# Performance work log

Measured on AMD Instinct MI355X. Metric: run time of the kernel, lower is better.

## Reference

```python
import jax, jax.numpy as jnp
import numpy as np

B, T, H = 32, 8192, 128

def setup_inputs() -> dict:
    key = jax.random.key(0)
    k1, k2, k3, k4, k5, k6 = jax.random.split(key, 6)
    stdv = 1.0 / np.sqrt(H)
    return {
        "hidden": jax.random.normal(k1, (B, H), jnp.float32),
        "encoder_outputs": jax.random.normal(k2, (T, B, H), jnp.float32),
        "len_seq": jax.random.randint(k3, (B,), 1, T + 1),  # valid lengths in [1, T]
        "W_attn": jax.random.normal(k4, (H, 2 * H), jnp.float32) * stdv,
        "b_attn": jnp.zeros((H,), jnp.float32),
        "v": jax.random.uniform(k5, (H,), jnp.float32, -stdv, stdv),
    }

def reference(hidden, encoder_outputs, len_seq, W_attn, b_attn, v):
    # hidden: [B,H]; encoder_outputs: [T,B,H]; len_seq: [B]
    T_ = encoder_outputs.shape[0]
    enc = jnp.transpose(encoder_outputs, (1, 0, 2))          # [B,T,H]
    h = jnp.broadcast_to(hidden[:, None, :], enc.shape)       # [B,T,H]
    # score(): relu(Linear(cat)) then v . energy
    energy = jax.nn.relu(jnp.concatenate([h, enc], axis=-1) @ W_attn.T + b_attn)  # [B,T,H]
    scores = jnp.einsum('bth,h->bt', energy, v)               # [B,T]
    # ragged masked softmax: softmax over first len_seq[i] positions, zeros after
    mask = jnp.arange(T_)[None, :] < len_seq[:, None]         # [B,T]
    attn = jax.nn.softmax(jnp.where(mask, scores, -jnp.inf), axis=1)
    attn = jnp.where(mask, attn, 0.0)
    return attn[:, None, :]                                   # [B,1,T]
```

## Files before the change

kernel.cpp:

```cpp
#include <hip/hip_runtime.h>
#include <hip/hip_bf16.h>

#define B 32
#define T 8192
#define H 128

typedef __attribute__((ext_vector_type(8)))  short short8_t;
typedef __attribute__((ext_vector_type(16))) float f32x16;

static __device__ __forceinline__ unsigned fbits(float x) { return __builtin_bit_cast(unsigned, x); }
static __device__ __forceinline__ float bfloat(unsigned u) { return __builtin_bit_cast(float, u); }

static __device__ __forceinline__ void pack4hi(const float4 f,
                                               unsigned& hi0, unsigned& hi1) {
    const unsigned u0 = fbits(f.x), u1 = fbits(f.y), u2 = fbits(f.z), u3 = fbits(f.w);
    hi0 = (u0 >> 16) | (u1 & 0xffff0000u);
    hi1 = (u2 >> 16) | (u3 & 0xffff0000u);
}

#define WPK_OFF  16384

__global__ void k_prep(const float* __restrict__ hidden,
                       const float* __restrict__ W_attn,
                       const float* __restrict__ b_attn,
                       float* __restrict__ u,
                       unsigned short* __restrict__ wpk) {
    const int tid = threadIdx.x;
    if (blockIdx.x < 32) {
        const int b = blockIdx.x;
        __shared__ float hrow[H];
        if (tid < H) hrow[tid] = hidden[b * H + tid];
        __syncthreads();
        if (tid < H) {
            const float* w = W_attn + (size_t)tid * (2 * H);
            float acc = b_attn[tid];
#pragma unroll
            for (int k = 0; k < H; ++k) acc = fmaf(w[k], hrow[k], acc);
            u[b * H + tid] = acc;
        }
    } else {
        const int idx  = (blockIdx.x - 32) * 256 + tid;
        const int s    = idx >> 8;
        const int m    = (idx >> 6) & 3;
        const int lane = idx & 63;
        const int h    = m * 32 + (lane & 31);
        const int k0   = s * 16 + (lane >> 5) * 8;
        const float* src = W_attn + (size_t)h * (2 * H) + H + k0;
        const int base = ((s * 4 + m) * 64 + lane) * 8;
#pragma unroll
        for (int e = 0; e < 8; ++e) {
            const float x = src[e];
            const unsigned ux = fbits(x);
            const unsigned hb = ux & 0xffff0000u;
            const float r = x - bfloat(hb);
            wpk[base + e]         = (unsigned short)(ux >> 16);
            wpk[16384 + base + e] = (unsigned short)(fbits(r) >> 16);
        }
    }
}

__global__ __launch_bounds__(512, 2) void k_scores_mfma(
    const float* __restrict__ enc,
    const float* __restrict__ u,
    const float* __restrict__ v,
    const unsigned short* __restrict__ wpk,
    float* __restrict__ scores)
{
    __shared__ uint2 hb[2][2048];
    __shared__ float cbuf[2][2][4][32];

    const int tid   = threadIdx.x;
    const int lane  = tid & 63;
    const int wid   = tid >> 6;
    const int tsel  = wid >> 2;
    const int mtile = wid & 3;
    const int l31   = lane & 31;
    const int kh    = lane >> 5;

    const int srow = tid >> 3;
    const int st8  = tid & 7;

    const int t0 = blockIdx.x * 32;
    const float4* enc4 = (const float4*)enc;

    short8_t w2hi[8], w2lo[8];
#pragma unroll
    for (int s = 0; s < 8; ++s) {
        const int fo = ((s * 4 + mtile) * 64 + lane) * 8;
        w2hi[s] = *(const short8_t*)(wpk + fo);
        w2lo[s] = *(const short8_t*)(wpk + 16384 + fo);
    }
    float4 uf[4], vv[4];
#pragma unroll
    for (int r4 = 0; r4 < 4; ++r4) {
        uf[r4] = *(const float4*)(u + l31 * H + mtile * 32 + r4 * 8 + kh * 4);
        vv[r4] = *(const float4*)(v + mtile * 32 + r4 * 8 + kh * 4);
    }

    float4 stg[4];
    {
        const float4* gs = enc4 + ((size_t)(t0 + 0) * 32 + srow) * 32;
#pragma unroll
        for (int i = 0; i < 4; ++i) stg[i] = gs[st8 + 8 * i];
#pragma unroll
        for (int i = 0; i < 4; ++i) {
            unsigned hi0, hi1;
            pack4hi(stg[i], hi0, hi1);
            const int p16 = st8 + 8 * i;
            const int idx = srow * 32 + (((p16 >> 1) + srow) & 15) * 2 + (p16 & 1);
            hb[0][idx] = make_uint2(hi0, hi1);
        }
        const float4* gs1 = enc4 + ((size_t)(t0 + 2) * 32 + srow) * 32;
#pragma unroll
        for (int i = 0; i < 4; ++i) stg[i] = gs1[st8 + 8 * i];
    }
    __syncthreads();

    const int rrow  = tsel * 32 + l31;
    const int rbase = rrow * 32;

#pragma unroll 1
    for (int q = 0; q < 16; ++q) {
        const int cur = q & 1, nxt = cur ^ 1;

        if (q < 15) {
#pragma unroll
            for (int i = 0; i < 4; ++i) {
                unsigned hi0, hi1;
                pack4hi(stg[i], hi0, hi1);
                const int p16 = st8 + 8 * i;
                const int idx = srow * 32 + (((p16 >> 1) + srow) & 15) * 2 + (p16 & 1);
                hb[nxt][idx] = make_uint2(hi0, hi1);
            }
        }
        if (q < 14) {
            const float4* gs = enc4 + ((size_t)(t0 + 2 * (q + 2)) * 32 + srow) * 32;
#pragma unroll
            for (int i = 0; i < 4; ++i) stg[i] = gs[st8 + 8 * i];
        }

        f32x16 acc;
#pragma unroll
        for (int r4 = 0; r4 < 4; ++r4) {
            acc[4 * r4 + 0] = uf[r4].x; acc[4 * r4 + 1] = uf[r4].y;
            acc[4 * r4 + 2] = uf[r4].z; acc[4 * r4 + 3] = uf[r4].w;
        }

#pragma unroll
        for (int s = 0; s < 8; ++s) {
            const int slot = (2 * s + kh + l31) & 15;
            const short8_t bh = *(const short8_t*)&hb[cur][rbase + slot * 2];
            acc = __builtin_amdgcn_mfma_f32_32x32x16_bf16(w2hi[s], bh, acc, 0, 0, 0);
            acc = __builtin_amdgcn_mfma_f32_32x32x16_bf16(w2lo[s], bh, acc, 0, 0, 0);
        }

        float psum = 0.f;
#pragma unroll
        for (int r4 = 0; r4 < 4; ++r4) {
            psum = fmaf(fmaxf(acc[4 * r4 + 0], 0.f), vv[r4].x, psum);
            psum = fmaf(fmaxf(acc[4 * r4 + 1], 0.f), vv[r4].y, psum);
            psum = fmaf(fmaxf(acc[4 * r4 + 2], 0.f), vv[r4].z, psum);
            psum = fmaf(fmaxf(acc[4 * r4 + 3], 0.f), vv[r4].w, psum);
        }
        psum += __shfl_xor(psum, 32);

        if (lane < 32) cbuf[cur][tsel][mtile][l31] = psum;

        __syncthreads();

        if (mtile == 0 && lane < 32) {
            const float r = cbuf[cur][tsel][0][l31] + cbuf[cur][tsel][1][l31]
                          + cbuf[cur][tsel][2][l31] + cbuf[cur][tsel][3][l31];
            scores[(size_t)l31 * T + (t0 + 2 * q + tsel)] = r;
        }
    }
}

#define SM_TPB 1024
#define SM_PER (T / SM_TPB)

__global__ __launch_bounds__(SM_TPB) void k_softmax(
    float* __restrict__ out, const int* __restrict__ len_seq)
{
    const int b    = blockIdx.x;
    const int tid  = threadIdx.x;
    const int lane = tid & 63;
    const int wid  = tid >> 6;
    const int len  = len_seq[b];
    float* s = out + (size_t)b * T;

    __shared__ float red[16];

    float val[SM_PER];
#pragma unroll
    for (int i = 0; i < SM_PER; ++i) val[i] = s[tid + i * SM_TPB];

    float m = -1e30f;
#pragma unroll
    for (int i = 0; i < SM_PER; ++i)
        if (tid + i * SM_TPB < len) m = fmaxf(m, val[i]);
#pragma unroll
    for (int off = 32; off >= 1; off >>= 1) m = fmaxf(m, __shfl_xor(m, off));
    if (lane == 0) red[wid] = m;
    __syncthreads();
    if (wid == 0) {
        float xv = (lane < 16) ? red[lane] : -1e30f;
#pragma unroll
        for (int off = 8; off >= 1; off >>= 1) xv = fmaxf(xv, __shfl_xor(xv, off));
        if (lane == 0) red[0] = xv;
    }
    __syncthreads();
    m = red[0];
    __syncthreads();

    float sum = 0.0f;
#pragma unroll
    for (int i = 0; i < SM_PER; ++i) {
        const int t = tid + i * SM_TPB;
        val[i] = (t < len) ? __expf(val[i] - m) : 0.0f;
        sum += val[i];
    }
#pragma unroll
    for (int off = 32; off >= 1; off >>= 1) sum += __shfl_xor(sum, off);
    if (lane == 0) red[wid] = sum;
    __syncthreads();
    if (wid == 0) {
        float xv = (lane < 16) ? red[lane] : 0.f;
#pragma unroll
        for (int off = 8; off >= 1; off >>= 1) xv += __shfl_xor(xv, off);
        if (lane == 0) red[0] = xv;
    }
    __syncthreads();
    const float inv = 1.0f / red[0];

#pragma unroll
    for (int i = 0; i < SM_PER; ++i) s[tid + i * SM_TPB] = val[i] * inv;
}

extern "C" void kernel_launch(void* const* d_in, const int* in_sizes, int n_in,
                              void* d_out, int out_size, void* d_ws, size_t ws_size,
                              hipStream_t stream) {
    const float* hidden = (const float*)d_in[0];
    const float* enc    = (const float*)d_in[1];
    const int*   len    = (const int*)d_in[2];
    const float* W      = (const float*)d_in[3];
    const float* bb     = (const float*)d_in[4];
    const float* v      = (const float*)d_in[5];

    float* out  = (float*)d_out;
    float* u_ws = (float*)d_ws;
    unsigned short* wpk = (unsigned short*)((char*)d_ws + WPK_OFF);

    k_prep<<<40, 256, 0, stream>>>(hidden, W, bb, u_ws, wpk);
    k_scores_mfma<<<256, 512, 0, stream>>>(enc, u_ws, v, wpk, out);
    k_softmax<<<B, SM_TPB, 0, stream>>>(out, len);
}
```

Measured before the change: 36.06 us.

## Fuse online softmax statistics into score kernel and widen final normalization grid

The score kernel now keeps running max and sum-of-exponentials per batch row (online softmax) for its time slice and writes per-block partials to workspace. A new final kernel merges the 256 partials per row and normalizes scores using 256 blocks instead of 32 large ones. This removes the separate max/sum reduction passes over the scores and spreads the final pass across more CUs. The cost is extra exp work inside the score loop, a serialized per-lane update, and a partial-merge step with extra exp calls.

```diff
diff --git a/kernel.cpp b/kernel.cpp
--- a/kernel.cpp
+++ b/kernel.cpp
@@ -19,6 +19,7 @@
 }
 
 #define WPK_OFF  16384
+#define PART_OFF 81920
 
 __global__ void k_prep(const float* __restrict__ hidden,
                        const float* __restrict__ W_attn,
@@ -64,10 +65,13 @@
     const float* __restrict__ u,
     const float* __restrict__ v,
     const unsigned short* __restrict__ wpk,
-    float* __restrict__ scores)
+    const int* __restrict__ len_seq,
+    float* __restrict__ scores,
+    float* __restrict__ part)
 {
     __shared__ uint2 hb[2][2048];
     __shared__ float cbuf[2][2][4][32];
+    __shared__ float pm[2][32], ps[2][32];
 
     const int tid   = threadIdx.x;
     const int lane  = tid & 63;
@@ -96,6 +100,7 @@
         uf[r4] = *(const float4*)(u + l31 * H + mtile * 32 + r4 * 8 + kh * 4);
         vv[r4] = *(const float4*)(v + mtile * 32 + r4 * 8 + kh * 4);
     }
+    const int lenb = len_seq[l31];
 
     float4 stg[4];
     {
@@ -118,6 +123,8 @@
 
     const int rrow  = tsel * 32 + l31;
     const int rbase = rrow * 32;
+
+    float m_run = -1e30f, s_run = 0.0f;
 
 #pragma unroll 1
     for (int q = 0; q < 16; ++q) {
@@ -171,70 +178,66 @@
         if (mtile == 0 && lane < 32) {
             const float r = cbuf[cur][tsel][0][l31] + cbuf[cur][tsel][1][l31]
                           + cbuf[cur][tsel][2][l31] + cbuf[cur][tsel][3][l31];
-            scores[(size_t)l31 * T + (t0 + 2 * q + tsel)] = r;
-        }
-    }
-}
-
-#define SM_TPB 1024
-#define SM_PER (T / SM_TPB)
-
-__global__ __launch_bounds__(SM_TPB) void k_softmax(
-    float* __restrict__ out, const int* __restrict__ len_seq)
+            const int t = t0 + 2 * q + tsel;
+            scores[(size_t)l31 * T + t] = r;
+            if (t < lenb) {
+                const float m_new = fmaxf(m_run, r);
+                s_run = s_run * __expf(m_run - m_new) + __expf(r - m_new);
+                m_run = m_new;
+            }
+        }
+    }
+
+    if (mtile == 0 && lane < 32) { pm[tsel][l31] = m_run; ps[tsel][l31] = s_run; }
+    __syncthreads();
+    if (tid < 32) {
+        const float m0 = pm[0][tid], m1 = pm[1][tid];
+        const float s0 = ps[0][tid], s1 = ps[1][tid];
+        const float M = fmaxf(m0, m1);
+        const float S = s0 * __expf(m0 - M) + s1 * __expf(m1 - M);
+        *(float2*)&part[((size_t)tid * 256 + blockIdx.x) * 2] = make_float2(M, S);
+    }
+}
+
+__global__ __launch_bounds__(256) void k_sm_final(
+    float* __restrict__ out,
+    const int* __restrict__ len_seq,
+    const float* __restrict__ part)
 {
-    const int b    = blockIdx.x;
+    const int b    = blockIdx.x >> 3;
+    const int c    = blockIdx.x & 7;
     const int tid  = threadIdx.x;
     const int lane = tid & 63;
     const int wid  = tid >> 6;
     const int len  = len_seq[b];
-    float* s = out + (size_t)b * T;
-
-    __shared__ float red[16];
-
-    float val[SM_PER];
-#pragma unroll
-    for (int i = 0; i < SM_PER; ++i) val[i] = s[tid + i * SM_TPB];
-
-    float m = -1e30f;
-#pragma unroll
-    for (int i = 0; i < SM_PER; ++i)
-        if (tid + i * SM_TPB < len) m = fmaxf(m, val[i]);
-#pragma unroll
-    for (int off = 32; off >= 1; off >>= 1) m = fmaxf(m, __shfl_xor(m, off));
-    if (lane == 0) red[wid] = m;
+
+    __shared__ float rm[4], rs[4];
+
+    float2 p = *(const float2*)&part[((size_t)b * 256 + tid) * 2];
+    float m = p.x, s = p.y;
+#pragma unroll
+    for (int off = 32; off >= 1; off >>= 1) {
+        const float m2 = __shfl_xor(m, off);
+        const float s2 = __shfl_xor(s, off);
+        const float M = fmaxf(m, m2);
+        s = s * __expf(m - M) + s2 * __expf(m2 - M);
+        m = M;
+    }
+    if (lane == 0) { rm[wid] = m; rs[wid] = s; }
     __syncthreads();
-    if (wid == 0) {
-        float xv = (lane < 16) ? red[lane] : -1e30f;
-#pragma unroll
-        for (int off = 8; off >= 1; off >>= 1) xv = fmaxf(xv, __shfl_xor(xv, off));
-        if (lane == 0) red[0] = xv;
-    }
-    __syncthreads();
-    m = red[0];
-    __syncthreads();
-
-    float sum = 0.0f;
-#pragma unroll
-    for (int i = 0; i < SM_PER; ++i) {
-        const int t = tid + i * SM_TPB;
-        val[i] = (t < len) ? __expf(val[i] - m) : 0.0f;
-        sum += val[i];
-    }
-#pragma unroll
-    for (int off = 32; off >= 1; off >>= 1) sum += __shfl_xor(sum, off);
-    if (lane == 0) red[wid] = sum;
-    __syncthreads();
-    if (wid == 0) {
-        float xv = (lane < 16) ? red[lane] : 0.f;
-#pragma unroll
-        for (int off = 8; off >= 1; off >>= 1) xv += __shfl_xor(xv, off);
-        if (lane == 0) red[0] = xv;
-    }
-    __syncthreads();
-    const float inv = 1.0f / red[0];
-
-#pragma unroll
-    for (int i = 0; i < SM_PER; ++i) s[tid + i * SM_TPB] = val[i] * inv;
+    const float M = fmaxf(fmaxf(rm[0], rm[1]), fmaxf(rm[2], rm[3]));
+    const float S = rs[0] * __expf(rm[0] - M) + rs[1] * __expf(rm[1] - M)
+                  + rs[2] * __expf(rm[2] - M) + rs[3] * __expf(rm[3] - M);
+    const float inv = 1.0f / S;
+
+    float* srow = out + (size_t)b * T + c * 1024;
+#pragma unroll
+    for (int i = 0; i < 4; ++i) {
+        const int tl = tid + i * 256;
+        const int t  = c * 1024 + tl;
+        const float x = srow[tl];
+        srow[tl] = (t < len) ? __expf(x - M) * inv : 0.0f;
+    }
 }
 
 extern "C" void kernel_launch(void* const* d_in, const int* in_sizes, int n_in,
@@ -250,8 +253,9 @@
     float* out  = (float*)d_out;
     float* u_ws = (float*)d_ws;
     unsigned short* wpk = (unsigned short*)((char*)d_ws + WPK_OFF);
+    float* part = (float*)((char*)d_ws + PART_OFF);
 
     k_prep<<<40, 256, 0, stream>>>(hidden, W, bb, u_ws, wpk);
-    k_scores_mfma<<<256, 512, 0, stream>>>(enc, u_ws, v, wpk, out);
-    k_softmax<<<B, SM_TPB, 0, stream>>>(out, len);
-}
+    k_scores_mfma<<<256, 512, 0, stream>>>(enc, u_ws, v, wpk, len, out, part);
+    k_sm_final<<<B * 8, 256, 0, stream>>>(out, len, part);
+}
```

Result: no change. 35.95 us (-0.3%).
